# Kernel optimization log

Measured on AMD Instinct MI355X. Metric: run time of the kernel, lower is better.

Reference implementation:

```python
import jax, jax.numpy as jnp
import numpy as np

N_NODES = 100000


def setup_inputs() -> dict:
    key = jax.random.key(0)
    k1, k2, k3 = jax.random.split(key, 3)
    x = jax.random.normal(k1, (N_NODES, 256), dtype=jnp.float32)
    edge_index = jax.random.randint(k2, (2, 1600000), 0, N_NODES, dtype=jnp.int64)
    W = jax.random.normal(k3, (256, 128), dtype=jnp.float32) * (1.0 / np.sqrt(256.0))
    b = jnp.zeros((128,), dtype=jnp.float32)
    alpha = jnp.full((128,), 0.25, dtype=jnp.float32)  # PReLU default init
    return {"x": x, "edge_index": edge_index, "W": W, "b": b, "alpha": alpha}


def reference(x, edge_index, W, b, alpha):
    N = x.shape[0]
    # --- GCNConv: add self-loops ---
    loops = jnp.arange(N, dtype=edge_index.dtype)
    row = jnp.concatenate([edge_index[0], loops])  # source nodes
    col = jnp.concatenate([edge_index[1], loops])  # destination nodes
    # symmetric normalization: deg computed at destinations (self-loops => deg >= 1)
    deg = jax.ops.segment_sum(jnp.ones(col.shape, x.dtype), col, num_segments=N)
    dinv = jax.lax.rsqrt(deg)
    norm = dinv[row] * dinv[col]  # [E+N]
    # linear transform then normalized scatter-add aggregation
    h = x @ W  # [N, H]
    msg = h[row] * norm[:, None]  # [E+N, H]
    out = jax.ops.segment_sum(msg, col, num_segments=N) + b  # bias after aggregation
    # --- PReLU (per-channel) ---
    return jnp.where(out >= 0, out, alpha * out)
```

## Files before the change

### kernel.cpp

```cpp
#include <hip/hip_runtime.h>

constexpr int KDIM = 256;
constexpr int HDIM = 128;
constexpr int GB   = 256;
constexpr int BK   = 128;

typedef __bf16 bf16x8 __attribute__((ext_vector_type(8)));
typedef float  f32x4  __attribute__((ext_vector_type(4)));

__device__ __forceinline__ ushort f2bf(float f) {
    unsigned u = __float_as_uint(f);
    unsigned r = (u + 0x7fffu + ((u >> 16) & 1u)) >> 16;
    return (ushort)r;
}

__device__ __forceinline__ void accum8(float* a, uint4 u) {
    a[0] += __uint_as_float(u.x << 16); a[1] += __uint_as_float(u.x & 0xffff0000u);
    a[2] += __uint_as_float(u.y << 16); a[3] += __uint_as_float(u.y & 0xffff0000u);
    a[4] += __uint_as_float(u.z << 16); a[5] += __uint_as_float(u.z & 0xffff0000u);
    a[6] += __uint_as_float(u.w << 16); a[7] += __uint_as_float(u.w & 0xffff0000u);
}

__global__ __launch_bounds__(256) void prep_c1_kernel(const float* __restrict__ W,
                                                      ushort* __restrict__ Wt,
                                                      ushort* __restrict__ hsb,
                                                      const int* __restrict__ col,
                                                      int* __restrict__ histG,
                                                      int n, int e, int nb, int chunk) {
    extern __shared__ int hist[];
    int b = blockIdx.x, t = threadIdx.x;
    if (b < 16) {
        int g = b * 256 + t;
        int lane = g & 63, cn = g >> 6;
        int c = cn >> 3, nf = cn & 7;
        int ncol = nf * 16 + (lane & 15);
        int k0 = c * 32 + (lane >> 4) * 8;
        ushort* dst = Wt + (size_t)g * 8;
        #pragma unroll
        for (int j = 0; j < 8; ++j) dst[j] = f2bf(W[(k0 + j) * HDIM + ncol]);
        return;
    }
    if (b == 16) {
        if (t < HDIM) hsb[(size_t)n * HDIM + t] = 0;
        return;
    }
    int g = b - 17;
    for (int i = t; i < nb; i += 256) hist[i] = 0;
    __syncthreads();
    int lo = g * chunk, hi = min(lo + chunk, e);
    for (int i = lo + t; i < hi; i += 256)
        atomicAdd(&hist[col[i] >> 7], 1);
    __syncthreads();
    for (int i = t; i < nb; i += 256) histG[i * GB + g] = hist[i];
}

__global__ __launch_bounds__(256) void scanA_kernel(const int* __restrict__ in,
                                                    int* __restrict__ partial, int n) {
    int t = threadIdx.x, base = blockIdx.x * 1024;
    int s = 0;
    #pragma unroll
    for (int j = 0; j < 4; ++j) {
        int i = base + j * 256 + t;
        if (i < n) s += in[i];
    }
    __shared__ int ws[4];
    #pragma unroll
    for (int d = 1; d < 64; d <<= 1) s += __shfl_xor(s, d, 64);
    int lane = t & 63, w = t >> 6;
    if (lane == 0) ws[w] = s;
    __syncthreads();
    if (t == 0) partial[blockIdx.x] = ws[0] + ws[1] + ws[2] + ws[3];
}

__global__ void scanB_kernel(int* __restrict__ partial, int nb) {
    int t = threadIdx.x;
    int v = (t < nb) ? partial[t] : 0;
    int orig = v;
    int lane = t & 63, w = t >> 6;
    #pragma unroll
    for (int d = 1; d < 64; d <<= 1) { int u = __shfl_up(v, d, 64); if (lane >= d) v += u; }
    __shared__ int ws[4];
    if (lane == 63) ws[w] = v;
    __syncthreads();
    int add = 0;
    #pragma unroll
    for (int i = 0; i < 4; ++i) if (i < w) add += ws[i];
    if (t < nb) partial[t] = v + add - orig;
}

__global__ __launch_bounds__(256) void scanC_kernel(const int* __restrict__ in,
                                                    const int* __restrict__ partial,
                                                    int* __restrict__ out, int n) {
    int t = threadIdx.x, base = blockIdx.x * 1024;
    int vals[4], tsum = 0;
    #pragma unroll
    for (int j = 0; j < 4; ++j) {
        int i = base + t * 4 + j;
        vals[j] = (i < n) ? in[i] : 0;
        tsum += vals[j];
    }
    int lane = t & 63, w = t >> 6;
    int incl = tsum;
    #pragma unroll
    for (int d = 1; d < 64; d <<= 1) { int u = __shfl_up(incl, d, 64); if (lane >= d) incl += u; }
    __shared__ int ws[4];
    if (lane == 63) ws[w] = incl;
    __syncthreads();
    int add = partial[blockIdx.x];
    #pragma unroll
    for (int i = 0; i < 4; ++i) if (i < w) add += ws[i];
    int run = add + incl - tsum;
    #pragma unroll
    for (int j = 0; j < 4; ++j) {
        int i = base + t * 4 + j;
        if (i < n) out[i] = run;
        run += vals[j];
    }
}

__global__ __launch_bounds__(256) void c3_place_kernel(const int* __restrict__ row,
                                                       const int* __restrict__ col,
                                                       const int* __restrict__ histS,
                                                       uint* __restrict__ ebuf,
                                                       int e, int nb, int chunk) {
    extern __shared__ int cur[];
    int g = blockIdx.x, t = threadIdx.x;
    for (int i = t; i < nb; i += 256) cur[i] = histS[i * GB + g];
    __syncthreads();
    int lo = g * chunk, hi = min(lo + chunk, e);
    for (int i = lo + t; i < hi; i += 256) {
        int c = col[i];
        int b = c >> 7;
        int pos = atomicAdd(&cur[b], 1);
        ebuf[pos] = ((uint)row[i] << 7) | (uint)(c & 127);
    }
}

__global__ __launch_bounds__(256) void fine_kernel(const int* __restrict__ histS,
                                                   uint* __restrict__ ebuf,
                                                   int* __restrict__ deg,
                                                   int* __restrict__ offs,
                                                   float* __restrict__ dinv,
                                                   int e, int nb, int n) {
    __shared__ uint elist[4096];
    __shared__ uint csrl[4096];
    __shared__ int hist[BK], excl[BK], cur[BK];
    int b = blockIdx.x, t = threadIdx.x;
    int seg0 = histS[b * GB];
    int seg1 = (b + 1 < nb) ? histS[(b + 1) * GB] : e;
    int cnt = min(seg1 - seg0, 4096);

    if (t < BK) { hist[t] = 0; cur[t] = 0; }
    __syncthreads();
    for (int i = t; i < cnt; i += 256) {
        uint v = ebuf[seg0 + i];
        elist[i] = v;
        atomicAdd(&hist[v & 127], 1);
    }
    __syncthreads();
    if (t < 64) {
        int v0 = hist[2 * t], v1 = hist[2 * t + 1];
        int s = v0 + v1, incl = s;
        #pragma unroll
        for (int d = 1; d < 64; d <<= 1) { int u = __shfl_up(incl, d, 64); if (t >= d) incl += u; }
        int base = incl - s;
        excl[2 * t] = base; excl[2 * t + 1] = base + v0;
    }
    __syncthreads();
    for (int i = t; i < cnt; i += 256) {
        uint v = elist[i];
        int d = v & 127;
        int r = atomicAdd(&cur[d], 1);
        csrl[excl[d] + r] = v >> 7;
    }
    __syncthreads();
    for (int i = t; i < cnt; i += 256) ebuf[seg0 + i] = csrl[i];
    if (t < BK) {
        int node = b * BK + t;
        if (node < n) {
            int dg = hist[t];
            deg[node]  = dg;
            offs[node] = seg0 + excl[t];
            dinv[node] = rsqrtf((float)(dg + 1));
        }
    }
}


constexpr int MT = 64;
constexpr int XS_STRIDE = 264;

__global__ __launch_bounds__(256) void gemm_kernel(const float* __restrict__ x,
                                                   const ushort* __restrict__ Wt,
                                                   const float* __restrict__ dinv,
                                                   ushort* __restrict__ hsb, int n) {
    __shared__ ushort xs[MT * XS_STRIDE];
    __shared__ float sdinv[MT];
    int t = threadIdx.x, lane = t & 63, w = t >> 6;
    int row0 = blockIdx.x * MT;

    bf16x8 bfrag[8][2];
    #pragma unroll
    for (int c = 0; c < 8; ++c)
        #pragma unroll
        for (int f = 0; f < 2; ++f)
            bfrag[c][f] = *(const bf16x8*)(Wt + (size_t)(((c * 8) + (w * 2 + f)) * 64 + lane) * 8);

    #pragma unroll
    for (int i = 0; i < 16; ++i) {
        int rl = w * 16 + i;
        int gr = row0 + rl; if (gr >= n) gr = n - 1;
        float4 v = *(const float4*)(x + (size_t)gr * KDIM + lane * 4);
        ushort4 o;
        o.x = f2bf(v.x); o.y = f2bf(v.y); o.z = f2bf(v.z); o.w = f2bf(v.w);
        *(ushort4*)(xs + rl * XS_STRIDE + lane * 4) = o;
    }
    if (t < MT) { int g = row0 + t; sdinv[t] = dinv[(g < n) ? g : (n - 1)]; }
    __syncthreads();

    #pragma unroll
    for (int s = 0; s < MT / 16; ++s) {
        f32x4 acc0 = {0.f, 0.f, 0.f, 0.f}, acc1 = {0.f, 0.f, 0.f, 0.f};
        #pragma unroll
        for (int c = 0; c < 8; ++c) {
            const ushort* ap = xs + (s * 16 + (lane & 15)) * XS_STRIDE + c * 32 + (lane >> 4) * 8;
            bf16x8 afrag = *(const bf16x8*)ap;
            acc0 = __builtin_amdgcn_mfma_f32_16x16x32_bf16(afrag, bfrag[c][0], acc0, 0, 0, 0);
            acc1 = __builtin_amdgcn_mfma_f32_16x16x32_bf16(afrag, bfrag[c][1], acc1, 0, 0, 0);
        }
        #pragma unroll
        for (int reg = 0; reg < 4; ++reg) {
            int rl = s * 16 + (lane >> 4) * 4 + reg;
            int gr = row0 + rl;
            if (gr < n) {
                float d = sdinv[rl];
                int col0 = w * 32 + (lane & 15);
                hsb[(size_t)gr * HDIM + col0]      = f2bf(acc0[reg] * d);
                hsb[(size_t)gr * HDIM + col0 + 16] = f2bf(acc1[reg] * d);
            }
        }
    }
}


__global__ __launch_bounds__(256) void aggregate_kernel(
    const ushort* __restrict__ hsb, const int* __restrict__ offs,
    const int* __restrict__ deg, const int* __restrict__ csr,
    const float* __restrict__ dinv, const float* __restrict__ b,
    const float* __restrict__ alpha, float* __restrict__ out, int n) {
    int wv = threadIdx.x >> 6, lane = threadIdx.x & 63;
    int node = blockIdx.x * 4 + wv;
    if (node >= n) return;
    int base = offs[node], cnt = deg[node];
    int slot = lane >> 4, chg = lane & 15;
    const uint4* hs4 = (const uint4*)hsb;

    float a[8];
    #pragma unroll
    for (int i = 0; i < 8; ++i) a[i] = 0.f;

    if (slot == 0) {
        uint4 u = hs4[(size_t)node * 16 + chg];
        accum8(a, u);
    }

    for (int j = 0; j < cnt; j += 64) {
        int m = min(cnt - j, 64);
        int idx = (lane < m) ? csr[base + j + lane] : n;
        for (int g = 0; g < m; g += 16) {
            int s0 = __shfl(idx, g + slot, 64);
            int s1 = __shfl(idx, g + 4 + slot, 64);
            int s2 = __shfl(idx, g + 8 + slot, 64);
            int s3 = __shfl(idx, g + 12 + slot, 64);
            uint4 u0 = hs4[(size_t)s0 * 16 + chg];
            uint4 u1 = hs4[(size_t)s1 * 16 + chg];
            uint4 u2 = hs4[(size_t)s2 * 16 + chg];
            uint4 u3 = hs4[(size_t)s3 * 16 + chg];
            accum8(a, u0); accum8(a, u1); accum8(a, u2); accum8(a, u3);
        }
    }

    #pragma unroll
    for (int i = 0; i < 8; ++i) {
        a[i] += __shfl_xor(a[i], 16, 64);
        a[i] += __shfl_xor(a[i], 32, 64);
    }

    if (slot == 0) {
        float dc = dinv[node];
        int c0 = chg * 8;
        float o[8];
        #pragma unroll
        for (int i = 0; i < 8; ++i) {
            float v = fmaf(dc, a[i], b[c0 + i]);
            o[i] = v >= 0.f ? v : alpha[c0 + i] * v;
        }
        float* op = out + (size_t)node * HDIM + c0;
        *(float4*)op       = make_float4(o[0], o[1], o[2], o[3]);
        *(float4*)(op + 4) = make_float4(o[4], o[5], o[6], o[7]);
    }
}


extern "C" void kernel_launch(void* const* d_in, const int* in_sizes, int n_in,
                              void* d_out, int out_size, void* d_ws, size_t ws_size,
                              hipStream_t stream) {
    const float* x     = (const float*)d_in[0];
    const int*   ei    = (const int*)d_in[1];
    const float* W     = (const float*)d_in[2];
    const float* b     = (const float*)d_in[3];
    const float* alpha = (const float*)d_in[4];
    float* out = (float*)d_out;

    int E = in_sizes[1] / 2;
    int N = in_sizes[0] / KDIM;
    int NB = (N + BK - 1) / BK;
    int SCAN_N = NB * GB;
    int chunk = (E + GB - 1) / GB;

    ushort* hsb  = (ushort*)d_ws;
    ushort* Wt   = hsb + (size_t)(N + 1) * HDIM;
    float* dinv  = (float*)(Wt + 32768);
    int* degG    = (int*)(dinv + N);
    int* offs    = degG + SCAN_N;
    int* histS   = offs + N;
    int* partial = histS + SCAN_N;
    uint* ebuf   = (uint*)(partial + 512);

    const int* rowp = ei;
    const int* colp = ei + E;

    int nbScan = (SCAN_N + 1023) / 1024;
    size_t ldsNB = (size_t)NB * sizeof(int);

    hipLaunchKernelGGL(prep_c1_kernel, dim3(17 + GB), dim3(256), ldsNB, stream,
                       W, Wt, hsb, colp, degG, N, E, NB, chunk);
    hipLaunchKernelGGL(scanA_kernel, dim3(nbScan), dim3(256), 0, stream, degG, partial, SCAN_N);
    hipLaunchKernelGGL(scanB_kernel, dim3(1), dim3(256), 0, stream, partial, nbScan);
    hipLaunchKernelGGL(scanC_kernel, dim3(nbScan), dim3(256), 0, stream, degG, partial, histS, SCAN_N);
    hipLaunchKernelGGL(c3_place_kernel, dim3(GB), dim3(256), ldsNB, stream, rowp, colp, histS, ebuf, E, NB, chunk);
    hipLaunchKernelGGL(fine_kernel,  dim3(NB), dim3(256), 0, stream, histS, ebuf, degG, offs, dinv, E, NB, N);
    hipLaunchKernelGGL(gemm_kernel,  dim3((N + MT - 1) / MT), dim3(256), 0, stream, x, Wt, dinv, hsb, N);
    hipLaunchKernelGGL(aggregate_kernel, dim3((N + 3) / 4), dim3(256), 0, stream,
                       hsb, offs, degG, (const int*)ebuf, dinv, b, alpha, out, N);
}
```

Baseline: 338.3 us.

## Fuse bucket placement into histogram pass with LDS-local sort per edge chunk

The histogram kernel now also sorts each 8192-edge chunk by coarse bucket in shared memory and writes it out contiguously, recording per-chunk local offsets. This removes the separate placement kernel, which did a second pass over row and col with scattered global writes. The fine kernel then gathers each bucket's segments from every chunk with serial per-thread copy loops into LDS before the local CSR sort. The trade-off is more chunks (about 196 instead of 256 blocks but a larger SCAN_N layout) and a fine-kernel gather that is serial per chunk and may be uneven.

```diff
diff --git a/kernel.cpp b/kernel.cpp
--- a/kernel.cpp
+++ b/kernel.cpp
@@ -1,9 +1,10 @@
 #include <hip/hip_runtime.h>
 
-constexpr int KDIM = 256;
-constexpr int HDIM = 128;
-constexpr int GB   = 256;
-constexpr int BK   = 128;
+constexpr int KDIM  = 256;
+constexpr int HDIM  = 128;
+constexpr int BK    = 128;
+constexpr int CHUNK = 8192;
+constexpr int NBMAX = 800;
 
 typedef __bf16 bf16x8 __attribute__((ext_vector_type(8)));
 typedef float  f32x4  __attribute__((ext_vector_type(4)));
@@ -21,13 +22,11 @@
     a[6] += __uint_as_float(u.w << 16); a[7] += __uint_as_float(u.w & 0xffff0000u);
 }
 
-__global__ __launch_bounds__(256) void prep_c1_kernel(const float* __restrict__ W,
-                                                      ushort* __restrict__ Wt,
-                                                      ushort* __restrict__ hsb,
-                                                      const int* __restrict__ col,
-                                                      int* __restrict__ histG,
-                                                      int n, int e, int nb, int chunk) {
-    extern __shared__ int hist[];
+__global__ __launch_bounds__(256) void prep_sort_kernel(
+    const float* __restrict__ W, ushort* __restrict__ Wt, ushort* __restrict__ hsb,
+    const int* __restrict__ row, const int* __restrict__ col,
+    uint* __restrict__ ebuf, int* __restrict__ histG, int* __restrict__ localOff,
+    int n, int e, int nbv, int gblk) {
     int b = blockIdx.x, t = threadIdx.x;
     if (b < 16) {
         int g = b * 256 + t;
@@ -45,13 +44,50 @@
         return;
     }
     int g = b - 17;
-    for (int i = t; i < nb; i += 256) hist[i] = 0;
-    __syncthreads();
-    int lo = g * chunk, hi = min(lo + chunk, e);
+    __shared__ uint dst[CHUNK];
+    __shared__ int hist[NBMAX], excl[NBMAX], cur[NBMAX];
+    __shared__ int ws2[4];
+    int lane = t & 63, w = t >> 6;
+    for (int i = t; i < nbv; i += 256) hist[i] = 0;
+    __syncthreads();
+    int lo = g * CHUNK, hi = min(lo + CHUNK, e);
     for (int i = lo + t; i < hi; i += 256)
         atomicAdd(&hist[col[i] >> 7], 1);
     __syncthreads();
-    for (int i = t; i < nb; i += 256) histG[i * GB + g] = hist[i];
+    {
+        int b0 = t * 4;
+        int h[4]; int s = 0;
+        #pragma unroll
+        for (int j = 0; j < 4; ++j) { h[j] = (b0 + j < nbv) ? hist[b0 + j] : 0; s += h[j]; }
+        int incl = s;
+        #pragma unroll
+        for (int d = 1; d < 64; d <<= 1) { int u = __shfl_up(incl, d, 64); if (lane >= d) incl += u; }
+        if (lane == 63) ws2[w] = incl;
+        __syncthreads();
+        int add = 0;
+        #pragma unroll
+        for (int i = 0; i < 4; ++i) if (i < w) add += ws2[i];
+        int run = add + incl - s;
+        #pragma unroll
+        for (int j = 0; j < 4; ++j) {
+            if (b0 + j < nbv) { excl[b0 + j] = run; cur[b0 + j] = run; }
+            run += h[j];
+        }
+    }
+    __syncthreads();
+    for (int i = lo + t; i < hi; i += 256) {
+        int c = col[i];
+        int bk = c >> 7;
+        int p = atomicAdd(&cur[bk], 1);
+        dst[p] = ((uint)row[i] << 7) | (uint)(c & 127);
+    }
+    __syncthreads();
+    int cnt = hi - lo;
+    for (int i = t; i < cnt; i += 256) ebuf[lo + i] = dst[i];
+    for (int i = t; i < nbv; i += 256) {
+        histG[i * gblk + g]    = hist[i];
+        localOff[i * gblk + g] = excl[i];
+    }
 }
 
 __global__ __launch_bounds__(256) void scanA_kernel(const int* __restrict__ in,
@@ -118,45 +154,32 @@
     }
 }
 
-__global__ __launch_bounds__(256) void c3_place_kernel(const int* __restrict__ row,
-                                                       const int* __restrict__ col,
-                                                       const int* __restrict__ histS,
-                                                       uint* __restrict__ ebuf,
-                                                       int e, int nb, int chunk) {
-    extern __shared__ int cur[];
-    int g = blockIdx.x, t = threadIdx.x;
-    for (int i = t; i < nb; i += 256) cur[i] = histS[i * GB + g];
-    __syncthreads();
-    int lo = g * chunk, hi = min(lo + chunk, e);
-    for (int i = lo + t; i < hi; i += 256) {
-        int c = col[i];
-        int b = c >> 7;
-        int pos = atomicAdd(&cur[b], 1);
-        ebuf[pos] = ((uint)row[i] << 7) | (uint)(c & 127);
-    }
-}
-
-__global__ __launch_bounds__(256) void fine_kernel(const int* __restrict__ histS,
-                                                   uint* __restrict__ ebuf,
+__global__ __launch_bounds__(256) void fine_kernel(const uint* __restrict__ ebuf,
+                                                   const int* __restrict__ histG,
+                                                   const int* __restrict__ localOff,
+                                                   const int* __restrict__ histS,
+                                                   uint* __restrict__ csr,
                                                    int* __restrict__ deg,
                                                    int* __restrict__ offs,
                                                    float* __restrict__ dinv,
-                                                   int e, int nb, int n) {
+                                                   int e, int nbv, int gblk, int n) {
     __shared__ uint elist[4096];
     __shared__ uint csrl[4096];
     __shared__ int hist[BK], excl[BK], cur[BK];
     int b = blockIdx.x, t = threadIdx.x;
-    int seg0 = histS[b * GB];
-    int seg1 = (b + 1 < nb) ? histS[(b + 1) * GB] : e;
+    int seg0 = histS[b * gblk];
+    int seg1 = (b + 1 < nbv) ? histS[(b + 1) * gblk] : e;
     int cnt = min(seg1 - seg0, 4096);
 
     if (t < BK) { hist[t] = 0; cur[t] = 0; }
-    __syncthreads();
-    for (int i = t; i < cnt; i += 256) {
-        uint v = ebuf[seg0 + i];
-        elist[i] = v;
-        atomicAdd(&hist[v & 127], 1);
-    }
+    for (int g = t; g < gblk; g += 256) {
+        int c   = histG[b * gblk + g];
+        int src = g * CHUNK + localOff[b * gblk + g];
+        int dst = histS[b * gblk + g] - seg0;
+        for (int i = 0; i < c; ++i) elist[dst + i] = ebuf[src + i];
+    }
+    __syncthreads();
+    for (int i = t; i < cnt; i += 256) atomicAdd(&hist[elist[i] & 127], 1);
     __syncthreads();
     if (t < 64) {
         int v0 = hist[2 * t], v1 = hist[2 * t + 1];
@@ -174,7 +197,7 @@
         csrl[excl[d] + r] = v >> 7;
     }
     __syncthreads();
-    for (int i = t; i < cnt; i += 256) ebuf[seg0 + i] = csrl[i];
+    for (int i = t; i < cnt; i += 256) csr[seg0 + i] = csrl[i];
     if (t < BK) {
         int node = b * BK + t;
         if (node < n) {
@@ -266,7 +289,7 @@
 
     for (int j = 0; j < cnt; j += 64) {
         int m = min(cnt - j, 64);
-        int idx = (lane < m) ? csr[base + j + lane] : n;
+        int idx = (lane < m) ? (int)csr[base + j + lane] : n;
         for (int g = 0; g < m; g += 16) {
             int s0 = __shfl(idx, g + slot, 64);
             int s1 = __shfl(idx, g + 4 + slot, 64);
@@ -315,32 +338,34 @@
     int E = in_sizes[1] / 2;
     int N = in_sizes[0] / KDIM;
     int NB = (N + BK - 1) / BK;
-    int SCAN_N = NB * GB;
-    int chunk = (E + GB - 1) / GB;
-
-    ushort* hsb  = (ushort*)d_ws;
-    ushort* Wt   = hsb + (size_t)(N + 1) * HDIM;
-    float* dinv  = (float*)(Wt + 32768);
-    int* degG    = (int*)(dinv + N);
-    int* offs    = degG + SCAN_N;
-    int* histS   = offs + N;
-    int* partial = histS + SCAN_N;
-    uint* ebuf   = (uint*)(partial + 512);
+    int GBLK = (E + CHUNK - 1) / CHUNK;
+    int SCAN_N = NB * GBLK;
+
+    ushort* hsb   = (ushort*)d_ws;
+    ushort* Wt    = hsb + (size_t)(N + 1) * HDIM;
+    float* dinv   = (float*)(Wt + 32768);
+    int* deg      = (int*)(dinv + N);
+    int* offs     = deg + N;
+    int* histG    = offs + N;
+    int* localOff = histG + SCAN_N;
+    int* histS    = localOff + SCAN_N;
+    int* partial  = histS + SCAN_N;
+    uint* ebuf    = (uint*)(partial + 512);
+    uint* csr     = ebuf + (size_t)GBLK * CHUNK;
 
     const int* rowp = ei;
     const int* colp = ei + E;
 
     int nbScan = (SCAN_N + 1023) / 1024;
-    size_t ldsNB = (size_t)NB * sizeof(int);
-
-    hipLaunchKernelGGL(prep_c1_kernel, dim3(17 + GB), dim3(256), ldsNB, stream,
-                       W, Wt, hsb, colp, degG, N, E, NB, chunk);
-    hipLaunchKernelGGL(scanA_kernel, dim3(nbScan), dim3(256), 0, stream, degG, partial, SCAN_N);
+
+    hipLaunchKernelGGL(prep_sort_kernel, dim3(17 + GBLK), dim3(256), 0, stream,
+                       W, Wt, hsb, rowp, colp, ebuf, histG, localOff, N, E, NB, GBLK);
+    hipLaunchKernelGGL(scanA_kernel, dim3(nbScan), dim3(256), 0, stream, histG, partial, SCAN_N);
     hipLaunchKernelGGL(scanB_kernel, dim3(1), dim3(256), 0, stream, partial, nbScan);
-    hipLaunchKernelGGL(scanC_kernel, dim3(nbScan), dim3(256), 0, stream, degG, partial, histS, SCAN_N);
-    hipLaunchKernelGGL(c3_place_kernel, dim3(GB), dim3(256), ldsNB, stream, rowp, colp, histS, ebuf, E, NB, chunk);
-    hipLaunchKernelGGL(fine_kernel,  dim3(NB), dim3(256), 0, stream, histS, ebuf, degG, offs, dinv, E, NB, N);
-    hipLaunchKernelGGL(gemm_kernel,  dim3((N + MT - 1) / MT), dim3(256), 0, stream, x, Wt, dinv, hsb, N);
+    hipLaunchKernelGGL(scanC_kernel, dim3(nbScan), dim3(256), 0, stream, histG, partial, histS, SCAN_N);
+    hipLaunchKernelGGL(fine_kernel, dim3(NB), dim3(256), 0, stream,
+                       ebuf, histG, localOff, histS, csr, deg, offs, dinv, E, NB, GBLK, N);
+    hipLaunchKernelGGL(gemm_kernel, dim3((N + MT - 1) / MT), dim3(256), 0, stream, x, Wt, dinv, hsb, N);
     hipLaunchKernelGGL(aggregate_kernel, dim3((N + 3) / 4), dim3(256), 0, stream,
-                       hsb, offs, degG, (const int*)ebuf, dinv, b, alpha, out, N);
-}
+                       hsb, offs, deg, (const int*)csr, dinv, b, alpha, out, N);
+}
```

Result: no change. 334.0 us (-1.3%).
